# Kernel optimization log

Hardware: AMD Instinct MI355X
Metric: run time of the kernel (lower is better)

The kernel has to match this reference:

```python
import jax, jax.numpy as jnp
import numpy as np
from jax import lax

B, C, W, H = 4, 64, 128, 128
K = 9            # snake kernel length
OC = 64          # out channels
EXTEND_SCOPE = 1.0
EPS = 1e-5
DN = ('NCHW', 'OIHW', 'NCHW')


def setup_inputs() -> dict:
    key = jax.random.key(0)
    ks = jax.random.split(key, 4)
    f = jax.random.normal(ks[0], (B, C, W, H), jnp.float32)
    offset_w = jax.random.normal(ks[1], (2 * K, C, 3, 3), jnp.float32) * 0.05
    offset_b = jnp.zeros((2 * K,), jnp.float32)
    bn_gamma = jnp.ones((2 * K,), jnp.float32)
    bn_beta = jnp.zeros((2 * K,), jnp.float32)
    bn_mean = jnp.zeros((2 * K,), jnp.float32)
    bn_var = jnp.ones((2 * K,), jnp.float32)
    conv_w = jax.random.normal(ks[2], (OC, C, K, 1), jnp.float32) * 0.05
    conv_b = jnp.zeros((OC,), jnp.float32)
    gn_gamma = jnp.ones((OC,), jnp.float32)
    gn_beta = jnp.zeros((OC,), jnp.float32)
    return dict(f=f, offset_w=offset_w, offset_b=offset_b, bn_gamma=bn_gamma,
                bn_beta=bn_beta, bn_mean=bn_mean, bn_var=bn_var,
                conv_w=conv_w, conv_b=conv_b, gn_gamma=gn_gamma, gn_beta=gn_beta)


def _dsconv(f, offset_w, offset_b, bn_gamma, bn_beta, bn_mean, bn_var,
            conv_w, conv_b, gn_gamma, gn_beta):
    # 1) offset branch: 3x3 conv -> BN (eval) -> tanh
    off = lax.conv_general_dilated(f, offset_w, (1, 1), 'SAME', dimension_numbers=DN)
    off = off + offset_b[None, :, None, None]
    off = (off - bn_mean[None, :, None, None]) * lax.rsqrt(bn_var + EPS)[None, :, None, None]
    off = off * bn_gamma[None, :, None, None] + bn_beta[None, :, None, None]
    off = jnp.tanh(off)
    y_off = off[:, :K]                      # [B,K,W,H]  (morph==0 uses y offsets)

    # 2) cumulative offset recurrence outward from the kernel center.
    # NOTE: indices 0 and K-1 keep their raw (non-accumulated) offsets,
    # exactly reproducing the original loop `for i in range(1, center)`.
    c = K // 2
    offs = [y_off[:, k] for k in range(K)]  # each [B,W,H]
    new = list(offs)
    new[c] = jnp.zeros_like(offs[c])
    for i in range(1, c):
        new[c + i] = new[c + i - 1] + offs[c + i]
        new[c - i] = new[c - i + 1] + offs[c - i]
    y_cum = jnp.stack(new, axis=1)          # [B,K,W,H]

    # 3) sampling coordinates (morph==0): y = row index + accumulated offset,
    # x = col index + linspace(-K//2, K//2, K) (python floor-div semantics).
    lin = jnp.linspace((-K) // 2, K // 2, K).astype(f.dtype)      # [-5..4] for K=9
    y = jnp.arange(W, dtype=f.dtype)[None, None, :, None] + y_cum * EXTEND_SCOPE
    x = jnp.broadcast_to(jnp.arange(H, dtype=f.dtype)[None, None, None, :]
                         + lin[None, :, None, None], (B, K, W, H))
    # layout [B, K*W, H] with row index = w*K + k
    ys = jnp.transpose(y, (0, 2, 1, 3)).reshape(B, K * W, H)
    xs = jnp.transpose(x, (0, 2, 1, 3)).reshape(B, K * W, H)

    # 4) bilinear gather from f (NCHW -> BWHC for channel-last gathers)
    y0 = jnp.clip(jnp.floor(ys).astype(jnp.int32), 0, W - 1)
    y1 = jnp.clip(y0 + 1, 0, W - 1)
    x0 = jnp.clip(jnp.floor(xs).astype(jnp.int32), 0, H - 1)
    x1 = jnp.clip(x0 + 1, 0, H - 1)
    fb = jnp.transpose(f, (0, 2, 3, 1))                  # [B,W,H,C]
    gather = jax.vmap(lambda fm, yy, xx: fm[yy, xx])     # -> [B,K*W,H,C]
    va0 = gather(fb, y0, x0)
    va1 = gather(fb, y0, x1)
    vb0 = gather(fb, y1, x0)
    vb1 = gather(fb, y1, x1)
    y0f, y1f = y0.astype(f.dtype), y1.astype(f.dtype)
    x0f, x1f = x0.astype(f.dtype), x1.astype(f.dtype)
    out = (va0 * ((y1f - ys) * (x1f - xs))[..., None]
           + va1 * ((y1f - ys) * (xs - x0f))[..., None]
           + vb0 * ((ys - y0f) * (x1f - xs))[..., None]
           + vb1 * ((ys - y0f) * (xs - x0f))[..., None])
    deformed = jnp.transpose(out, (0, 3, 1, 2))          # [B,C,K*W,H]

    # 5) (K,1)-strided conv collapses the K snake samples -> [B,OC,W,H]
    z = lax.conv_general_dilated(deformed, conv_w, (K, 1), 'VALID', dimension_numbers=DN)
    z = z + conv_b[None, :, None, None]

    # 6) GroupNorm(OC//4 groups) + ReLU
    G = OC // 4
    zg = z.reshape(B, G, OC // G, W, H)
    mu = zg.mean(axis=(2, 3, 4), keepdims=True)
    var = zg.var(axis=(2, 3, 4), keepdims=True)
    zg = (zg - mu) * lax.rsqrt(var + EPS)
    z = zg.reshape(B, OC, W, H) * gn_gamma[None, :, None, None] + gn_beta[None, :, None, None]
    return jax.nn.relu(z)


def reference(f, offset_w, offset_b, bn_gamma, bn_beta, bn_mean, bn_var,
              conv_w, conv_b, gn_gamma, gn_beta):
    return _dsconv(f, offset_w, offset_b, bn_gamma, bn_beta, bn_mean, bn_var,
                   conv_w, conv_b, gn_gamma, gn_beta)
```

## Files before the change

### kernel.cpp

```cpp
#include <hip/hip_runtime.h>
#include <hip/hip_bf16.h>

#define EPSV 1e-5f

typedef __attribute__((ext_vector_type(8))) short short8;
typedef __attribute__((ext_vector_type(4))) float f32x4;

__device__ __forceinline__ void gl_lds16(const void* g, void* l) {
    __builtin_amdgcn_global_load_lds(
        (const __attribute__((address_space(1))) unsigned int*)g,
        (__attribute__((address_space(3))) unsigned int*)l, 16, 0, 0);
}

__device__ __forceinline__ unsigned int bl2(unsigned int a, unsigned int b,
                                            unsigned int c, unsigned int d,
                                            float w00, float w01, float w10, float w11) {
    float lo = __uint_as_float(a << 16) * w00 + __uint_as_float(b << 16) * w01
             + __uint_as_float(c << 16) * w10 + __uint_as_float(d << 16) * w11;
    float hi = __uint_as_float(a & 0xffff0000u) * w00 + __uint_as_float(b & 0xffff0000u) * w01
             + __uint_as_float(c & 0xffff0000u) * w10 + __uint_as_float(d & 0xffff0000u) * w11;
    return ((unsigned int)__bfloat16_as_ushort(__float2bfloat16(lo)))
         | (((unsigned int)__bfloat16_as_ushort(__float2bfloat16(hi))) << 16);
}

__device__ __forceinline__ unsigned int pk2(float a, float b) {
    return ((unsigned int)__bfloat16_as_ushort(__float2bfloat16(a)))
         | (((unsigned int)__bfloat16_as_ushort(__float2bfloat16(b))) << 16);
}

__global__ __launch_bounds__(256) void k_pre(const float* __restrict__ f,
                                             const float* __restrict__ cw,
                                             const float* __restrict__ ow,
                                             ushort* __restrict__ fbh,
                                             ushort* __restrict__ flo,
                                             ushort* __restrict__ wpk,
                                             ushort* __restrict__ wpk2,
                                             float* __restrict__ stats) {
    int blk = blockIdx.x;
    int t = threadIdx.x;
    if (blk < 1024) {
        __shared__ float tile[64][65];
        int xt = blk & 1;
        int y  = (blk >> 1) & 127;
        int b  = blk >> 8;
        int x = t & 63, c0 = t >> 6;
        const float* src = f + (((size_t)b * 64) * 128 + y) * 128 + xt * 64;
#pragma unroll
        for (int i = 0; i < 64; i += 4)
            tile[c0 + i][x] = src[(size_t)(c0 + i) * 16384 + x];
        __syncthreads();
        size_t dbase = (((size_t)b * 128 + y) * 128 + xt * 64) * 64;
        int cc = t & 63, x0 = t >> 6;
#pragma unroll
        for (int i = 0; i < 64; i += 4) {
            float v = tile[cc][x0 + i];
            ushort hi = __bfloat16_as_ushort(__float2bfloat16(v));
            float vhi = __uint_as_float((unsigned int)hi << 16);
            ushort lo = __bfloat16_as_ushort(__float2bfloat16(v - vhi));
            fbh[dbase + (size_t)(x0 + i) * 64 + cc] = hi;
            flo[dbase + (size_t)(x0 + i) * 64 + cc] = lo;
        }
    } else if (blk < 1168) {
        int idx = (blk - 1024) * 256 + t;
        int j  = idx & 7;
        int l  = (idx >> 3) & 63;
        int ot = (idx >> 9) & 3;
        int kk = (idx >> 11) & 1;
        int k  = idx >> 12;
        int c  = kk * 32 + ((l >> 4) << 3) + j;
        int oc = (ot << 4) + (l & 15);
        wpk[idx] = __bfloat16_as_ushort(__float2bfloat16(cw[((size_t)oc * 64 + c) * 9 + k]));
        if (idx < 128) stats[idx] = 0.f;
    } else {
        int idx = (blk - 1168) * 256 + t;
        int j   = idx & 7;
        int l   = (idx >> 3) & 63;
        int kk  = (idx >> 9) & 1;
        int tap = idx >> 10;
        int c   = kk * 32 + ((l >> 4) << 3) + j;
        int n   = l & 15;
        float v = (n < 9) ? ow[((size_t)n * 64 + c) * 9 + tap] : 0.f;
        ushort hi = __bfloat16_as_ushort(__float2bfloat16(v));
        float vhi = __uint_as_float((unsigned int)hi << 16);
        ushort lo = __bfloat16_as_ushort(__float2bfloat16(v - vhi));
        wpk2[idx] = hi;
        wpk2[idx + 9216] = lo;
    }
}

__global__ __launch_bounds__(256, 3) void k_fused(
    const ushort* __restrict__ fbh,
    const ushort* __restrict__ flo,
    const ushort* __restrict__ wpk,
    const ushort* __restrict__ wpk2,
    const float* __restrict__ ob, const float* __restrict__ bng,
    const float* __restrict__ bnb, const float* __restrict__ bnm,
    const float* __restrict__ bnv, const float* __restrict__ cb,
    ushort* __restrict__ z, float* __restrict__ stats)
{
    __shared__ union {
        struct {
            ushort win[24192];
            float  tup[9][32][4];
        } p;
        float Z2[32 * 65];
    } sm;
    __shared__ float redS[16], redQ[16];

    int jb = blockIdx.x;
    int orig = (jb & 7) * 256 + (jb >> 3);
    int hq = orig & 3;
    int w  = (orig >> 2) & 127;
    int b  = orig >> 9;
    int h0 = hq << 5;
    int t    = threadIdx.x;
    int lane = t & 63;
    int wid  = t >> 6;
    int m = wid & 1;
    int n = wid >> 1;
    const char* winb = (const char*)sm.p.win;

#pragma unroll
    for (int p = 0; p < 12; ++p) {
        if (p == 11 && t >= 208) break;
        int ib = p * 4096 + t * 16;
        int ri = ib / 5376;
        int wb = ib - ri * 5376;
        int dys = ri < 3 ? ri + 3 : (ri < 6 ? ri - 3 : ri);
        int grow = min(max(w + dys - 4, 0), 127);
        int colIdx = wb >> 7;
        int c16 = (wb >> 4) & 7;
        int gcol = min(max(h0 - 5 + colIdx, 0), 127);
        int sch = c16 ^ (colIdx & 7);
        const ushort* src = fbh + ((((size_t)b << 7) + grow) * 128 + gcol) * 64 + (sch << 3);
        gl_lds16(src, (void*)(winb + ib));
    }
    asm volatile("s_waitcnt vmcnt(8)" ::: "memory");
    __builtin_amdgcn_sched_barrier(0);
    __syncthreads();

    if (wid < 2) {
        f32x4 acck = {0.f, 0.f, 0.f, 0.f};
        const short8* wp2 = (const short8*)wpk2;
        int px0 = (m << 4) + (lane & 15);
        int q = lane >> 4;
#pragma unroll
        for (int tap = 0; tap < 9; ++tap) {
            int dy = tap / 3, dx = tap - dy * 3;
            int ysrc = w + dy - 1;
            if ((unsigned)ysrc < 128u) {
                int col = h0 + px0 + dx - 1;
                bool ok = (unsigned)col < 128u;
                int xslot = px0 + dx + 4;
                int rbase = dy * 5376 + (xslot << 7);
                uint4 h0v = *(const uint4*)(winb + rbase + ((q ^ (xslot & 7)) << 4));
                uint4 h1v = *(const uint4*)(winb + rbase + (((q + 4) ^ (xslot & 7)) << 4));
                int colc = min(max(col, 0), 127);
                const ushort* lsrc = flo + ((((size_t)b << 7) + ysrc) * 128 + colc) * 64 + (q << 3);
                uint4 l0v = *(const uint4*)lsrc;
                uint4 l1v = *(const uint4*)(lsrc + 32);
                if (!ok) {
                    h0v = make_uint4(0, 0, 0, 0); h1v = make_uint4(0, 0, 0, 0);
                    l0v = make_uint4(0, 0, 0, 0); l1v = make_uint4(0, 0, 0, 0);
                }
                short8 wh0 = wp2[(tap * 2 + 0) * 64 + lane];
                short8 wh1 = wp2[(tap * 2 + 1) * 64 + lane];
                short8 wl0 = wp2[1152 + (tap * 2 + 0) * 64 + lane];
                short8 wl1 = wp2[1152 + (tap * 2 + 1) * 64 + lane];
                short8 ah0 = *(short8*)&h0v, ah1 = *(short8*)&h1v;
                short8 al0 = *(short8*)&l0v, al1 = *(short8*)&l1v;
                acck = __builtin_amdgcn_mfma_f32_16x16x32_bf16(ah0, wh0, acck, 0, 0, 0);
                acck = __builtin_amdgcn_mfma_f32_16x16x32_bf16(al0, wh0, acck, 0, 0, 0);
                acck = __builtin_amdgcn_mfma_f32_16x16x32_bf16(ah0, wl0, acck, 0, 0, 0);
                acck = __builtin_amdgcn_mfma_f32_16x16x32_bf16(ah1, wh1, acck, 0, 0, 0);
                acck = __builtin_amdgcn_mfma_f32_16x16x32_bf16(al1, wh1, acck, 0, 0, 0);
                acck = __builtin_amdgcn_mfma_f32_16x16x32_bf16(ah1, wl1, acck, 0, 0, 0);
            }
        }
        float* csm = (float*)sm.p.tup;
#pragma unroll
        for (int r = 0; r < 4; ++r) {
            int pxo = (m << 4) + ((lane >> 4) << 2) + r;
            int ko = lane & 15;
            if (ko < 9) csm[pxo * 9 + ko] = acck[r];
        }
    }
    asm volatile("s_waitcnt vmcnt(0)" ::: "memory");
    __syncthreads();

    if (t < 32) {
        const float* csm = (const float*)sm.p.tup;
        float tk[9];
#pragma unroll
        for (int k = 0; k < 9; ++k) {
            float zz = csm[t * 9 + k] + ob[k];
            zz = (zz - bnm[k]) * rsqrtf(bnv[k] + EPSV);
            zz = zz * bng[k] + bnb[k];
            tk[k] = tanhf(zz);
        }
        float nw_[9];
        nw_[4] = 0.f;
        nw_[5] = tk[5];
        nw_[6] = nw_[5] + tk[6];
        nw_[7] = nw_[6] + tk[7];
        nw_[8] = tk[8];
        nw_[3] = tk[3];
        nw_[2] = nw_[3] + tk[2];
        nw_[1] = nw_[2] + tk[1];
        nw_[0] = tk[0];
#pragma unroll
        for (int k = 0; k < 9; ++k) {
            float ys = (float)w + nw_[k];
            int y0 = min(max((int)floorf(ys), 0), 127);
            int y1 = min(y0 + 1, 127);
            float wy0 = (float)y1 - ys, wy1 = ys - (float)y0;
            int d0 = min(max(y0 - w + 4, 0), 8);
            int d1 = min(max(y1 - w + 4, 0), 8);
            int p0 = d0 < 3 ? d0 + 3 : (d0 < 6 ? d0 - 3 : d0);
            int p1 = d1 < 3 ? d1 + 3 : (d1 < 6 ? d1 - 3 : d1);
            float4 tv;
            tv.x = wy0; tv.y = wy1;
            tv.z = __int_as_float(p0 * 5376);
            tv.w = __int_as_float(p1 * 5376);
            *(float4*)sm.p.tup[k][t] = tv;
        }
    }
    __syncthreads();

    f32x4 acc0 = {0.f, 0.f, 0.f, 0.f};
    f32x4 acc1 = {0.f, 0.f, 0.f, 0.f};
    const short8* wp8 = (const short8*)wpk;
    int px = (lane & 15) + (m << 4);
    int q  = lane >> 4;
    float fpx = (float)(h0 + px);
#pragma unroll 3
    for (int k = 0; k < 9; ++k) {
        float4 tv = *(const float4*)sm.p.tup[k][px];
        float xs = fpx + (-5.0f + 1.125f * (float)k);
        int x0 = min(max((int)floorf(xs), 0), 127);
        int x1 = min(x0 + 1, 127);
        float wx0 = (float)x1 - xs;
        float wx1 = xs - (float)x0;
        float w00 = tv.x * wx0, w01 = tv.x * wx1, w10 = tv.y * wx0, w11 = tv.y * wx1;
        int rb0 = __float_as_int(tv.z), rb1 = __float_as_int(tv.w);
        int cx0 = x0 - h0 + 5, cx1 = x1 - h0 + 5;
        int s00 = rb0 + (cx0 << 7), s01 = rb0 + (cx1 << 7);
        int s10 = rb1 + (cx0 << 7), s11 = rb1 + (cx1 << 7);
        int qa0 = (q ^ (cx0 & 7)) << 4,       qa1 = (q ^ (cx1 & 7)) << 4;
        int qb0 = ((q + 4) ^ (cx0 & 7)) << 4, qb1 = ((q + 4) ^ (cx1 & 7)) << 4;
        uint4 a00 = *(const uint4*)(winb + s00 + qa0);
        uint4 a01 = *(const uint4*)(winb + s01 + qa1);
        uint4 a10 = *(const uint4*)(winb + s10 + qa0);
        uint4 a11 = *(const uint4*)(winb + s11 + qa1);
        uint4 b00 = *(const uint4*)(winb + s00 + qb0);
        uint4 b01 = *(const uint4*)(winb + s01 + qb1);
        uint4 b10 = *(const uint4*)(winb + s10 + qb0);
        uint4 b11 = *(const uint4*)(winb + s11 + qb1);
        uint4 f0u, f1u;
        f0u.x = bl2(a00.x, a01.x, a10.x, a11.x, w00, w01, w10, w11);
        f0u.y = bl2(a00.y, a01.y, a10.y, a11.y, w00, w01, w10, w11);
        f0u.z = bl2(a00.z, a01.z, a10.z, a11.z, w00, w01, w10, w11);
        f0u.w = bl2(a00.w, a01.w, a10.w, a11.w, w00, w01, w10, w11);
        f1u.x = bl2(b00.x, b01.x, b10.x, b11.x, w00, w01, w10, w11);
        f1u.y = bl2(b00.y, b01.y, b10.y, b11.y, w00, w01, w10, w11);
        f1u.z = bl2(b00.z, b01.z, b10.z, b11.z, w00, w01, w10, w11);
        f1u.w = bl2(b00.w, b01.w, b10.w, b11.w, w00, w01, w10, w11);
        short8 af0 = *(short8*)&f0u, af1 = *(short8*)&f1u;
        int fb0 = (k * 8 + (n << 1)) * 64 + lane;
        short8 wf00 = wp8[fb0];
        short8 wf01 = wp8[fb0 + 64];
        short8 wf10 = wp8[fb0 + 256];
        short8 wf11 = wp8[fb0 + 320];
        acc0 = __builtin_amdgcn_mfma_f32_16x16x32_bf16(af0, wf00, acc0, 0, 0, 0);
        acc0 = __builtin_amdgcn_mfma_f32_16x16x32_bf16(af1, wf10, acc0, 0, 0, 0);
        acc1 = __builtin_amdgcn_mfma_f32_16x16x32_bf16(af0, wf01, acc1, 0, 0, 0);
        acc1 = __builtin_amdgcn_mfma_f32_16x16x32_bf16(af1, wf11, acc1, 0, 0, 0);
    }

    int lane15 = lane & 15;
    float b0 = cb[(n << 5) + lane15];
    float b1 = cb[(n << 5) + 16 + lane15];
    float v00 = acc0.x + b0, v01 = acc0.y + b0, v02 = acc0.z + b0, v03 = acc0.w + b0;
    float v10 = acc1.x + b1, v11 = acc1.y + b1, v12 = acc1.z + b1, v13 = acc1.w + b1;
    float s0 = v00 + v01 + v02 + v03;
    float q0 = v00 * v00 + v01 * v01 + v02 * v02 + v03 * v03;
    float s1 = v10 + v11 + v12 + v13;
    float q1 = v10 * v10 + v11 * v11 + v12 * v12 + v13 * v13;
    if (t < 16) { redS[t] = 0.f; redQ[t] = 0.f; }
    __syncthreads();
    float* Z2 = (float*)&sm;
    int g0 = (n << 3) + (lane15 >> 2);
    atomicAdd(&redS[g0], s0);     atomicAdd(&redQ[g0], q0);
    atomicAdd(&redS[g0 + 4], s1); atomicAdd(&redQ[g0 + 4], q1);
    int pxb = (m << 4) + ((lane >> 4) << 2);
    int ocb = (n << 5) + lane15;
    Z2[(pxb + 0) * 65 + ocb] = v00;
    Z2[(pxb + 1) * 65 + ocb] = v01;
    Z2[(pxb + 2) * 65 + ocb] = v02;
    Z2[(pxb + 3) * 65 + ocb] = v03;
    Z2[(pxb + 0) * 65 + ocb + 16] = v10;
    Z2[(pxb + 1) * 65 + ocb + 16] = v11;
    Z2[(pxb + 2) * 65 + ocb + 16] = v12;
    Z2[(pxb + 3) * 65 + ocb + 16] = v13;
    __syncthreads();
    if (t < 16) {
        atomicAdd(&stats[((size_t)b * 16 + t) * 2 + 0], redS[t]);
        atomicAdd(&stats[((size_t)b * 16 + t) * 2 + 1], redQ[t]);
    }
    int oc = t >> 2, part = t & 3;
    float o0x = Z2[(part * 8 + 0) * 65 + oc];
    float o0y = Z2[(part * 8 + 1) * 65 + oc];
    float o0z = Z2[(part * 8 + 2) * 65 + oc];
    float o0w = Z2[(part * 8 + 3) * 65 + oc];
    float o1x = Z2[(part * 8 + 4) * 65 + oc];
    float o1y = Z2[(part * 8 + 5) * 65 + oc];
    float o1z = Z2[(part * 8 + 6) * 65 + oc];
    float o1w = Z2[(part * 8 + 7) * 65 + oc];
    uint4 pk;
    pk.x = pk2(o0x, o0y);
    pk.y = pk2(o0z, o0w);
    pk.z = pk2(o1x, o1y);
    pk.w = pk2(o1z, o1w);
    ushort* zp = z + (((size_t)(b << 6) + oc) << 14) + (w << 7) + (hq << 5) + part * 8;
    *(uint4*)zp = pk;
}

__global__ __launch_bounds__(256) void k_gn(const ushort* __restrict__ z,
                                            const float* __restrict__ stats,
                                            const float* __restrict__ gg,
                                            const float* __restrict__ gb,
                                            float* __restrict__ out) {
    int idx = blockIdx.x * 256 + threadIdx.x;
    size_t base = (size_t)idx * 8;
    int oc = (int)((base >> 14) & 63);
    int b  = (int)(base >> 20);
    int g  = oc >> 2;
    float sm = stats[((size_t)b * 16 + g) * 2 + 0];
    float sq = stats[((size_t)b * 16 + g) * 2 + 1];
    const float cnt = 65536.f;
    float mu  = sm / cnt;
    float var = sq / cnt - mu * mu;
    float inv = rsqrtf(var + EPSV);
    float gam = gg[oc] * inv;
    float bet = gb[oc] - mu * gam;
    uint4 v = *(const uint4*)(z + base);
    float4 o0, o1;
    o0.x = fmaxf(__uint_as_float(v.x << 16) * gam + bet, 0.f);
    o0.y = fmaxf(__uint_as_float(v.x & 0xffff0000u) * gam + bet, 0.f);
    o0.z = fmaxf(__uint_as_float(v.y << 16) * gam + bet, 0.f);
    o0.w = fmaxf(__uint_as_float(v.y & 0xffff0000u) * gam + bet, 0.f);
    o1.x = fmaxf(__uint_as_float(v.z << 16) * gam + bet, 0.f);
    o1.y = fmaxf(__uint_as_float(v.z & 0xffff0000u) * gam + bet, 0.f);
    o1.z = fmaxf(__uint_as_float(v.w << 16) * gam + bet, 0.f);
    o1.w = fmaxf(__uint_as_float(v.w & 0xffff0000u) * gam + bet, 0.f);
    *(float4*)(out + base) = o0;
    *(float4*)(out + base + 4) = o1;
}

extern "C" void kernel_launch(void* const* d_in, const int* in_sizes, int n_in,
                              void* d_out, int out_size, void* d_ws, size_t ws_size,
                              hipStream_t stream) {
    const float* f   = (const float*)d_in[0];
    const float* ow  = (const float*)d_in[1];
    const float* ob  = (const float*)d_in[2];
    const float* bng = (const float*)d_in[3];
    const float* bnb = (const float*)d_in[4];
    const float* bnm = (const float*)d_in[5];
    const float* bnv = (const float*)d_in[6];
    const float* cw  = (const float*)d_in[7];
    const float* cb  = (const float*)d_in[8];
    const float* gg  = (const float*)d_in[9];
    const float* gb  = (const float*)d_in[10];

    char* wsb = (char*)d_ws;
    ushort* fbh  = (ushort*)wsb;
    ushort* flo  = (ushort*)(wsb + 8388608);
    ushort* wpk  = (ushort*)(wsb + 16777216);
    ushort* wpk2 = (ushort*)(wsb + 16850944);
    ushort* z    = (ushort*)(wsb + 16887808);
    float*  st   = (float*)(wsb + 25276416);

    k_pre<<<1204, 256, 0, stream>>>(f, cw, ow, fbh, flo, wpk, wpk2, st);
    k_fused<<<2048, 256, 0, stream>>>(fbh, flo, wpk, wpk2, ob, bng, bnb, bnm, bnv, cb, z, st);
    k_gn<<<2048, 256, 0, stream>>>(z, st, gg, gb, (float*)d_out);
}
```

Before: 162.9 us.

## Shrink LDS window to 7 rows and 41 cols, raise occupancy to 4 blocks

The shared-memory input window shrinks from 9 rows x 42 columns to 7 rows x 41 columns, and the per-tap interpolation table moves to separate wy0/wy1/packed-row-offset arrays. This cuts LDS per block so the launch bound can rise from 3 to 4 blocks per CU. The offset-conv loop now software-pipelines its loads one tap ahead and splits the MFMA chain across two accumulators to shorten the dependency chain. Sample rows are clamped to +-3 instead of +-4, which relies on the accumulated tanh offsets staying within that range and may change results for larger offsets.

```diff
diff --git a/kernel.cpp b/kernel.cpp
--- a/kernel.cpp
+++ b/kernel.cpp
@@ -44,10 +44,9 @@
         int y  = (blk >> 1) & 127;
         int b  = blk >> 8;
         int x = t & 63, c0 = t >> 6;
-        const float* src = f + (((size_t)b * 64) * 128 + y) * 128 + xt * 64;
 #pragma unroll
         for (int i = 0; i < 64; i += 4)
-            tile[c0 + i][x] = src[(size_t)(c0 + i) * 16384 + x];
+            tile[c0 + i][x] = f[(((size_t)b * 64 + c0 + i) * 128 + y) * 128 + xt * 64 + x];
         __syncthreads();
         size_t dbase = (((size_t)b * 128 + y) * 128 + xt * 64) * 64;
         int cc = t & 63, x0 = t >> 6;
@@ -88,7 +87,7 @@
     }
 }
 
-__global__ __launch_bounds__(256, 3) void k_fused(
+__global__ __launch_bounds__(256, 4) void k_fused(
     const ushort* __restrict__ fbh,
     const ushort* __restrict__ flo,
     const ushort* __restrict__ wpk,
@@ -98,14 +97,14 @@
     const float* __restrict__ bnv, const float* __restrict__ cb,
     ushort* __restrict__ z, float* __restrict__ stats)
 {
-    __shared__ union {
-        struct {
-            ushort win[24192];
-            float  tup[9][32][4];
-        } p;
-        float Z2[32 * 65];
-    } sm;
-    __shared__ float redS[16], redQ[16];
+    __shared__ struct {
+        ushort win[18368];
+        float  wy0a[288];
+        float  wy1a[288];
+        unsigned int rowsa[288];
+        float  redS[16];
+        float  redQ[16];
+    } smx;
 
     int jb = blockIdx.x;
     int orig = (jb & 7) * 256 + (jb >> 3);
@@ -118,16 +117,16 @@
     int wid  = t >> 6;
     int m = wid & 1;
     int n = wid >> 1;
-    const char* winb = (const char*)sm.p.win;
-
-#pragma unroll
-    for (int p = 0; p < 12; ++p) {
-        if (p == 11 && t >= 208) break;
+    char* winb = (char*)smx.win;
+
+#pragma unroll
+    for (int p = 0; p < 9; ++p) {
+        if (p == 8 && t >= 248) break;
         int ib = p * 4096 + t * 16;
-        int ri = ib / 5376;
-        int wb = ib - ri * 5376;
-        int dys = ri < 3 ? ri + 3 : (ri < 6 ? ri - 3 : ri);
-        int grow = min(max(w + dys - 4, 0), 127);
+        int ri = ib / 5248;
+        int wb = ib - ri * 5248;
+        int dy = ri < 3 ? ri - 1 : (ri < 5 ? ri - 6 : ri - 3);
+        int grow = min(max(w + dy, 0), 127);
         int colIdx = wb >> 7;
         int c16 = (wb >> 4) & 7;
         int gcol = min(max(h0 - 5 + colIdx, 0), 127);
@@ -135,61 +134,71 @@
         const ushort* src = fbh + ((((size_t)b << 7) + grow) * 128 + gcol) * 64 + (sch << 3);
         gl_lds16(src, (void*)(winb + ib));
     }
-    asm volatile("s_waitcnt vmcnt(8)" ::: "memory");
+    asm volatile("s_waitcnt vmcnt(5)" ::: "memory");
     __builtin_amdgcn_sched_barrier(0);
     __syncthreads();
 
     if (wid < 2) {
-        f32x4 acck = {0.f, 0.f, 0.f, 0.f};
+        f32x4 accA = {0.f, 0.f, 0.f, 0.f};
+        f32x4 accB = {0.f, 0.f, 0.f, 0.f};
         const short8* wp2 = (const short8*)wpk2;
         int px0 = (m << 4) + (lane & 15);
         int q = lane >> 4;
+        uint4 z4 = make_uint4(0u, 0u, 0u, 0u);
+        uint4 ch0, ch1, cl0, cl1, nh0, nh1, nl0, nl1;
+
+#define LOADT(TAP, H0, H1, L0, L1)                                              \
+        {                                                                       \
+            int dy_ = (TAP) / 3, dx_ = (TAP) - dy_ * 3;                         \
+            int ysrc_ = w + dy_ - 1;                                            \
+            int col_ = h0 + px0 + dx_ - 1;                                      \
+            bool ok_ = ((unsigned)col_ < 128u) && ((unsigned)ysrc_ < 128u);     \
+            int xslot_ = px0 + dx_ + 4;                                         \
+            int rbase_ = dy_ * 5248 + (xslot_ << 7);                            \
+            H0 = *(const uint4*)(winb + rbase_ + ((q ^ (xslot_ & 7)) << 4));    \
+            H1 = *(const uint4*)(winb + rbase_ + (((q + 4) ^ (xslot_ & 7)) << 4)); \
+            int colc_ = min(max(col_, 0), 127);                                 \
+            int ysc_ = min(max(ysrc_, 0), 127);                                 \
+            const ushort* lsrc_ = flo + ((((size_t)b << 7) + ysc_) * 128 + colc_) * 64 + (q << 3); \
+            L0 = *(const uint4*)lsrc_;                                          \
+            L1 = *(const uint4*)(lsrc_ + 32);                                   \
+            if (!ok_) { H0 = z4; H1 = z4; L0 = z4; L1 = z4; }                   \
+        }
+
+        LOADT(0, ch0, ch1, cl0, cl1);
 #pragma unroll
         for (int tap = 0; tap < 9; ++tap) {
-            int dy = tap / 3, dx = tap - dy * 3;
-            int ysrc = w + dy - 1;
-            if ((unsigned)ysrc < 128u) {
-                int col = h0 + px0 + dx - 1;
-                bool ok = (unsigned)col < 128u;
-                int xslot = px0 + dx + 4;
-                int rbase = dy * 5376 + (xslot << 7);
-                uint4 h0v = *(const uint4*)(winb + rbase + ((q ^ (xslot & 7)) << 4));
-                uint4 h1v = *(const uint4*)(winb + rbase + (((q + 4) ^ (xslot & 7)) << 4));
-                int colc = min(max(col, 0), 127);
-                const ushort* lsrc = flo + ((((size_t)b << 7) + ysrc) * 128 + colc) * 64 + (q << 3);
-                uint4 l0v = *(const uint4*)lsrc;
-                uint4 l1v = *(const uint4*)(lsrc + 32);
-                if (!ok) {
-                    h0v = make_uint4(0, 0, 0, 0); h1v = make_uint4(0, 0, 0, 0);
-                    l0v = make_uint4(0, 0, 0, 0); l1v = make_uint4(0, 0, 0, 0);
-                }
-                short8 wh0 = wp2[(tap * 2 + 0) * 64 + lane];
-                short8 wh1 = wp2[(tap * 2 + 1) * 64 + lane];
-                short8 wl0 = wp2[1152 + (tap * 2 + 0) * 64 + lane];
-                short8 wl1 = wp2[1152 + (tap * 2 + 1) * 64 + lane];
-                short8 ah0 = *(short8*)&h0v, ah1 = *(short8*)&h1v;
-                short8 al0 = *(short8*)&l0v, al1 = *(short8*)&l1v;
-                acck = __builtin_amdgcn_mfma_f32_16x16x32_bf16(ah0, wh0, acck, 0, 0, 0);
-                acck = __builtin_amdgcn_mfma_f32_16x16x32_bf16(al0, wh0, acck, 0, 0, 0);
-                acck = __builtin_amdgcn_mfma_f32_16x16x32_bf16(ah0, wl0, acck, 0, 0, 0);
-                acck = __builtin_amdgcn_mfma_f32_16x16x32_bf16(ah1, wh1, acck, 0, 0, 0);
-                acck = __builtin_amdgcn_mfma_f32_16x16x32_bf16(al1, wh1, acck, 0, 0, 0);
-                acck = __builtin_amdgcn_mfma_f32_16x16x32_bf16(ah1, wl1, acck, 0, 0, 0);
-            }
-        }
-        float* csm = (float*)sm.p.tup;
+            if (tap < 8) LOADT(tap + 1, nh0, nh1, nl0, nl1);
+            short8 wh0 = wp2[(tap * 2 + 0) * 64 + lane];
+            short8 wh1 = wp2[(tap * 2 + 1) * 64 + lane];
+            short8 wl0 = wp2[1152 + (tap * 2 + 0) * 64 + lane];
+            short8 wl1 = wp2[1152 + (tap * 2 + 1) * 64 + lane];
+            short8 ah0 = *(short8*)&ch0, ah1 = *(short8*)&ch1;
+            short8 al0 = *(short8*)&cl0, al1 = *(short8*)&cl1;
+            accA = __builtin_amdgcn_mfma_f32_16x16x32_bf16(ah0, wh0, accA, 0, 0, 0);
+            accB = __builtin_amdgcn_mfma_f32_16x16x32_bf16(ah1, wh1, accB, 0, 0, 0);
+            accA = __builtin_amdgcn_mfma_f32_16x16x32_bf16(al0, wh0, accA, 0, 0, 0);
+            accB = __builtin_amdgcn_mfma_f32_16x16x32_bf16(al1, wh1, accB, 0, 0, 0);
+            accA = __builtin_amdgcn_mfma_f32_16x16x32_bf16(ah0, wl0, accA, 0, 0, 0);
+            accB = __builtin_amdgcn_mfma_f32_16x16x32_bf16(ah1, wl1, accB, 0, 0, 0);
+            ch0 = nh0; ch1 = nh1; cl0 = nl0; cl1 = nl1;
+        }
+#undef LOADT
+        float* csm = smx.wy0a;
 #pragma unroll
         for (int r = 0; r < 4; ++r) {
             int pxo = (m << 4) + ((lane >> 4) << 2) + r;
             int ko = lane & 15;
-            if (ko < 9) csm[pxo * 9 + ko] = acck[r];
+            if (ko < 9) csm[pxo * 9 + ko] = accA[r] + accB[r];
         }
     }
     asm volatile("s_waitcnt vmcnt(0)" ::: "memory");
     __syncthreads();
 
+    float wy0r[9], wy1r[9];
+    unsigned int pkr[9];
     if (t < 32) {
-        const float* csm = (const float*)sm.p.tup;
+        const float* csm = smx.wy0a;
         float tk[9];
 #pragma unroll
         for (int k = 0; k < 9; ++k) {
@@ -213,16 +222,22 @@
             float ys = (float)w + nw_[k];
             int y0 = min(max((int)floorf(ys), 0), 127);
             int y1 = min(y0 + 1, 127);
-            float wy0 = (float)y1 - ys, wy1 = ys - (float)y0;
-            int d0 = min(max(y0 - w + 4, 0), 8);
-            int d1 = min(max(y1 - w + 4, 0), 8);
-            int p0 = d0 < 3 ? d0 + 3 : (d0 < 6 ? d0 - 3 : d0);
-            int p1 = d1 < 3 ? d1 + 3 : (d1 < 6 ? d1 - 3 : d1);
-            float4 tv;
-            tv.x = wy0; tv.y = wy1;
-            tv.z = __int_as_float(p0 * 5376);
-            tv.w = __int_as_float(p1 * 5376);
-            *(float4*)sm.p.tup[k][t] = tv;
+            wy0r[k] = (float)y1 - ys;
+            wy1r[k] = ys - (float)y0;
+            int s0 = min(max(y0 - w + 3, 0), 6);
+            int s1 = min(max(y1 - w + 3, 0), 6);
+            int p0 = (s0 >= 2 && s0 <= 4) ? (s0 - 2) : ((s0 < 2) ? (s0 + 3) : s0);
+            int p1 = (s1 >= 2 && s1 <= 4) ? (s1 - 2) : ((s1 < 2) ? (s1 + 3) : s1);
+            pkr[k] = (unsigned int)(p0 * 5248) | ((unsigned int)(p1 * 5248) << 16);
+        }
+    }
+    __syncthreads();
+    if (t < 32) {
+#pragma unroll
+        for (int k = 0; k < 9; ++k) {
+            smx.wy0a[k * 32 + t]  = wy0r[k];
+            smx.wy1a[k * 32 + t]  = wy1r[k];
+            smx.rowsa[k * 32 + t] = pkr[k];
         }
     }
     __syncthreads();
@@ -235,27 +250,31 @@
     float fpx = (float)(h0 + px);
 #pragma unroll 3
     for (int k = 0; k < 9; ++k) {
-        float4 tv = *(const float4*)sm.p.tup[k][px];
+        float wy0 = smx.wy0a[k * 32 + px];
+        float wy1 = smx.wy1a[k * 32 + px];
+        unsigned int pkw = smx.rowsa[k * 32 + px];
+        int rb0 = (int)(pkw & 0xffffu);
+        int rb1 = (int)(pkw >> 16);
         float xs = fpx + (-5.0f + 1.125f * (float)k);
         int x0 = min(max((int)floorf(xs), 0), 127);
         int x1 = min(x0 + 1, 127);
         float wx0 = (float)x1 - xs;
         float wx1 = xs - (float)x0;
-        float w00 = tv.x * wx0, w01 = tv.x * wx1, w10 = tv.y * wx0, w11 = tv.y * wx1;
-        int rb0 = __float_as_int(tv.z), rb1 = __float_as_int(tv.w);
-        int cx0 = x0 - h0 + 5, cx1 = x1 - h0 + 5;
-        int s00 = rb0 + (cx0 << 7), s01 = rb0 + (cx1 << 7);
-        int s10 = rb1 + (cx0 << 7), s11 = rb1 + (cx1 << 7);
-        int qa0 = (q ^ (cx0 & 7)) << 4,       qa1 = (q ^ (cx1 & 7)) << 4;
-        int qb0 = ((q + 4) ^ (cx0 & 7)) << 4, qb1 = ((q + 4) ^ (cx1 & 7)) << 4;
-        uint4 a00 = *(const uint4*)(winb + s00 + qa0);
-        uint4 a01 = *(const uint4*)(winb + s01 + qa1);
-        uint4 a10 = *(const uint4*)(winb + s10 + qa0);
-        uint4 a11 = *(const uint4*)(winb + s11 + qa1);
-        uint4 b00 = *(const uint4*)(winb + s00 + qb0);
-        uint4 b01 = *(const uint4*)(winb + s01 + qb1);
-        uint4 b10 = *(const uint4*)(winb + s10 + qb0);
-        uint4 b11 = *(const uint4*)(winb + s11 + qb1);
+        float w00 = wy0 * wx0, w01 = wy0 * wx1, w10 = wy1 * wx0, w11 = wy1 * wx1;
+        int cx0 = min(x0 - h0 + 5, 40);
+        int cx1 = min(cx0 + 1, 40);
+        int qa0 = (q ^ (cx0 & 7)) << 4;
+        int qa1 = (q ^ (cx1 & 7)) << 4;
+        int s00 = rb0 + (cx0 << 7) + qa0, s01 = rb0 + (cx1 << 7) + qa1;
+        int s10 = rb1 + (cx0 << 7) + qa0, s11 = rb1 + (cx1 << 7) + qa1;
+        uint4 a00 = *(const uint4*)(winb + s00);
+        uint4 a01 = *(const uint4*)(winb + s01);
+        uint4 a10 = *(const uint4*)(winb + s10);
+        uint4 a11 = *(const uint4*)(winb + s11);
+        uint4 b00 = *(const uint4*)(winb + (s00 ^ 64));
+        uint4 b01 = *(const uint4*)(winb + (s01 ^ 64));
+        uint4 b10 = *(const uint4*)(winb + (s10 ^ 64));
+        uint4 b11 = *(const uint4*)(winb + (s11 ^ 64));
         uint4 f0u, f1u;
         f0u.x = bl2(a00.x, a01.x, a10.x, a11.x, w00, w01, w10, w11);
         f0u.y = bl2(a00.y, a01.y, a10.y, a11.y, w00, w01, w10, w11);
@@ -286,12 +305,12 @@
     float q0 = v00 * v00 + v01 * v01 + v02 * v02 + v03 * v03;
     float s1 = v10 + v11 + v12 + v13;
     float q1 = v10 * v10 + v11 * v11 + v12 * v12 + v13 * v13;
-    if (t < 16) { redS[t] = 0.f; redQ[t] = 0.f; }
-    __syncthreads();
-    float* Z2 = (float*)&sm;
+    if (t < 16) { smx.redS[t] = 0.f; smx.redQ[t] = 0.f; }
+    __syncthreads();
+    float* Z2 = (float*)&smx;
     int g0 = (n << 3) + (lane15 >> 2);
-    atomicAdd(&redS[g0], s0);     atomicAdd(&redQ[g0], q0);
-    atomicAdd(&redS[g0 + 4], s1); atomicAdd(&redQ[g0 + 4], q1);
+    atomicAdd(&smx.redS[g0], s0);     atomicAdd(&smx.redQ[g0], q0);
+    atomicAdd(&smx.redS[g0 + 4], s1); atomicAdd(&smx.redQ[g0 + 4], q1);
     int pxb = (m << 4) + ((lane >> 4) << 2);
     int ocb = (n << 5) + lane15;
     Z2[(pxb + 0) * 65 + ocb] = v00;
@@ -304,8 +323,8 @@
     Z2[(pxb + 3) * 65 + ocb + 16] = v13;
     __syncthreads();
     if (t < 16) {
-        atomicAdd(&stats[((size_t)b * 16 + t) * 2 + 0], redS[t]);
-        atomicAdd(&stats[((size_t)b * 16 + t) * 2 + 1], redQ[t]);
+        atomicAdd(&stats[((size_t)b * 16 + t) * 2 + 0], smx.redS[t]);
+        atomicAdd(&stats[((size_t)b * 16 + t) * 2 + 1], smx.redQ[t]);
     }
     int oc = t >> 2, part = t & 3;
     float o0x = Z2[(part * 8 + 0) * 65 + oc];
```

Measured after the change: 157.5 us. 3.3% less time.
